# Kernel tuning notes

Hardware: AMD Instinct MI355X
Metric: run time of the kernel (lower is better)

The kernel has to match this reference:

```python
import jax, jax.numpy as jnp
import numpy as np

B = 1024
FEATURE_NUM = 13 + 26 * 4000  # 104013 (13 dense + 26 sparse fields, one-hot dim 4000 each)
FIELD_NUM = 13 + 26           # 39
K = 8


def setup_inputs() -> dict:
    key = jax.random.key(0)
    k1, k2, k3 = jax.random.split(key, 3)
    inputs = jax.random.uniform(k1, (B, FEATURE_NUM), dtype=jnp.float32)
    w0 = jnp.zeros((1,), dtype=jnp.float32)
    w = jax.random.normal(k2, (FEATURE_NUM, 1), dtype=jnp.float32) * 0.05
    v = jax.random.normal(k3, (FEATURE_NUM, FIELD_NUM, K), dtype=jnp.float32) * 0.05
    return {"inputs": inputs, "w0": w0, "w": w, "v": v}


def reference(inputs, w0, w, v):
    # linear part: [B, 1]
    linear_part = w0 + inputs @ w
    # field_f: [B, field_num, K] via tensordot over feature axis
    field_f = jnp.tensordot(inputs, v, axes=1)
    # sum over upper triangle (i<j) of <field_f_i, field_f_j> using the
    # sum-square FM identity: 0.5 * (||sum_i f_i||^2 - sum_i ||f_i||^2)
    s = field_f.sum(axis=1)                       # [B, K]
    inter = 0.5 * (jnp.sum(s * s, axis=-1)
                   - jnp.sum(field_f * field_f, axis=(1, 2)))  # [B]
    return linear_part + inter[:, None]           # [B, 1]
```

## Files before the change

kernel.cpp:

```cpp
#include <hip/hip_runtime.h>
#include <stdint.h>

#define B_SZ 1024
#define F_SZ 104013
#define NFIELD 39
#define N_RAW 312
#define N_PAD 320
#define KB_STEPS 3251
#define PART_ELEMS ((size_t)B_SZ * N_PAD)

using bf16x8 = __attribute__((ext_vector_type(8))) short;
using f32x4  = __attribute__((ext_vector_type(4))) float;

typedef __attribute__((address_space(3))) void* lds_vp;
typedef const __attribute__((address_space(1))) void* glb_cvp;

__device__ __forceinline__ void ld16(const void* g, void* l) {
  __builtin_amdgcn_global_load_lds((glb_cvp)g, (lds_vp)l, 16, 0, 0);
}

__device__ __forceinline__ unsigned int pack_bf16(float a, float b) {
  unsigned int ua = __float_as_uint(a) + 0x8000u;
  unsigned int ub = __float_as_uint(b) + 0x8000u;
  return (ua >> 16) | (ub & 0xffff0000u);
}

__global__ __launch_bounds__(256) void pack_v(const float* __restrict__ v,
                                              const float* __restrict__ w,
                                              uint4* __restrict__ Bp) {
  const int kb = blockIdx.x;
  const int t  = threadIdx.x;
  __shared__ float vs[32][324];

  for (int idx = t; idx < 32 * 78; idx += 256) {
    int r = idx / 78, c4 = (idx % 78) * 4;
    int k = kb * 32 + r;
    float4 val = make_float4(0.f, 0.f, 0.f, 0.f);
    if (k < F_SZ) val = *(const float4*)(v + (size_t)k * N_RAW + c4);
    *(float4*)&vs[r][c4] = val;
  }
  if (t < 32) {
    int k = kb * 32 + t;
    vs[t][312] = (k < F_SZ) ? w[k] : 0.f;
#pragma unroll
    for (int c = 313; c < 320; ++c) vs[t][c] = 0.f;
  }
  __syncthreads();

#pragma unroll
  for (int i = 0; i < 5; ++i) {
    int p  = t + 256 * i;
    int l  = p & 63;
    int kr = (l >> 4) * 8;
    int col = (p >> 6) * 16 + (l & 15);
    uint4 o;
    o.x = pack_bf16(vs[kr + 0][col], vs[kr + 1][col]);
    o.y = pack_bf16(vs[kr + 2][col], vs[kr + 3][col]);
    o.z = pack_bf16(vs[kr + 4][col], vs[kr + 5][col]);
    o.w = pack_bf16(vs[kr + 6][col], vs[kr + 7][col]);
    Bp[(size_t)kb * 1280 + p] = o;
  }
}

__global__ __launch_bounds__(256, 2) void gemm_split(const float* __restrict__ A,
                                                     const uint4* __restrict__ Bp,
                                                     float* __restrict__ part) {
  const int S  = gridDim.y;
  const int mt = blockIdx.x, s = blockIdx.y;
  const int t  = threadIdx.x;
  const int w  = t >> 6, l = t & 63;
  const int wr = w >> 1, wc = w & 1;
  const int lm = l & 15, lq = l >> 4;
  const int row0 = mt * 128;
  const int kb0 = (int)((long long)KB_STEPS * s / S);
  const int kb1 = (int)((long long)KB_STEPS * (s + 1) / S);

  __shared__ __align__(16) char smem[2][36864];

  const int lr  = l >> 3;
  const int kgl = ((l & 7) - lr) & 7;
  size_t arowbase[4];
#pragma unroll
  for (int j = 0; j < 4; ++j)
    arowbase[j] = (size_t)(row0 + (w * 4 + j) * 8 + lr) * F_SZ + (size_t)(kgl * 4);

  auto stage = [&](int kb, int buf, bool withA) {
    if (withA) {
#pragma unroll
      for (int j = 0; j < 4; ++j)
        ld16(A + arowbase[j] + (size_t)kb * 32, smem[buf] + (w * 4 + j) * 1024);
    }
#pragma unroll
    for (int j = 0; j < 5; ++j)
      ld16(Bp + ((size_t)kb * 20 + w * 5 + j) * 64 + l,
           smem[buf] + 16384 + (w * 5 + j) * 1024);
  };

  f32x4 acc[4][10];
#pragma unroll
  for (int i = 0; i < 4; ++i)
#pragma unroll
    for (int n = 0; n < 10; ++n) acc[i][n] = (f32x4)0.f;

  stage(kb0, 0, true);
  int cur = 0;
  for (int kb = kb0; kb < kb1; ++kb) {
    __syncthreads();
    if (kb + 1 < kb1) stage(kb + 1, cur ^ 1, (kb + 1) != KB_STEPS - 1);

    bf16x8 afrag[4];
    if (kb != KB_STEPS - 1) {
      const char* base = smem[cur];
      const int rot = lm & 7;
      const int p0 = (lq * 2 + rot) & 7;
      const int p1 = (lq * 2 + 1 + rot) & 7;
#pragma unroll
      for (int i = 0; i < 4; ++i) {
        int rowq = wr * 8 + i * 2 + (lm >> 3);
        f32x4 r0 = *(const f32x4*)(base + rowq * 1024 + rot * 128 + p0 * 16);
        f32x4 r1 = *(const f32x4*)(base + rowq * 1024 + rot * 128 + p1 * 16);
        uint4 pk = make_uint4(pack_bf16(r0[0], r0[1]), pack_bf16(r0[2], r0[3]),
                              pack_bf16(r1[0], r1[1]), pack_bf16(r1[2], r1[3]));
        afrag[i] = __builtin_bit_cast(bf16x8, pk);
      }
    } else {
      int kbase = kb * 32 + lq * 8;
#pragma unroll
      for (int i = 0; i < 4; ++i) {
        const float* ap = A + (size_t)(row0 + wr * 64 + i * 16 + lm) * F_SZ;
        float f[8];
#pragma unroll
        for (int jj = 0; jj < 8; ++jj)
          f[jj] = (kbase + jj < F_SZ) ? ap[kbase + jj] : 0.f;
        uint4 pk = make_uint4(pack_bf16(f[0], f[1]), pack_bf16(f[2], f[3]),
                              pack_bf16(f[4], f[5]), pack_bf16(f[6], f[7]));
        afrag[i] = __builtin_bit_cast(bf16x8, pk);
      }
    }

#pragma unroll
    for (int n = 0; n < 10; ++n) {
      bf16x8 bf = __builtin_bit_cast(
          bf16x8, *(const uint4*)(smem[cur] + 16384 + (wc * 10 + n) * 1024 + l * 16));
#pragma unroll
      for (int i = 0; i < 4; ++i)
        acc[i][n] = __builtin_amdgcn_mfma_f32_16x16x32_bf16(afrag[i], bf,
                                                            acc[i][n], 0, 0, 0);
    }
    cur ^= 1;
  }

  float* out = part + (size_t)s * PART_ELEMS;
#pragma unroll
  for (int i = 0; i < 4; ++i) {
    int rb = row0 + wr * 64 + i * 16 + lq * 4;
#pragma unroll
    for (int n = 0; n < 10; ++n) {
      int col = (wc * 10 + n) * 16 + lm;
#pragma unroll
      for (int r = 0; r < 4; ++r)
        out[(size_t)(rb + r) * N_PAD + col] = acc[i][n][r];
    }
  }
}

__global__ __launch_bounds__(256) void finalize(const float* __restrict__ part,
                                                const float* __restrict__ w0,
                                                float* __restrict__ out, int S) {
  const int b = blockIdx.x;
  const int t = threadIdx.x;
  __shared__ float crow[N_PAD];
  __shared__ float red[4];
  __shared__ float skl[8];

  for (int n = t; n < N_PAD; n += 256) {
    float acc = 0.f;
    for (int s = 0; s < S; ++s)
      acc += part[(size_t)s * PART_ELEMS + (size_t)b * N_PAD + n];
    crow[n] = acc;
  }
  __syncthreads();

  float sq = 0.f;
  for (int n = t; n < N_RAW; n += 256) sq += crow[n] * crow[n];
#pragma unroll
  for (int off = 32; off; off >>= 1) sq += __shfl_down(sq, off);
  if ((t & 63) == 0) red[t >> 6] = sq;
  if (t < 8) {
    float sk = 0.f;
#pragma unroll
    for (int f = 0; f < NFIELD; ++f) sk += crow[f * 8 + t];
    skl[t] = sk;
  }
  __syncthreads();
  if (t == 0) {
    float sumsq = red[0] + red[1] + red[2] + red[3];
    float ss = 0.f;
#pragma unroll
    for (int k = 0; k < 8; ++k) ss += skl[k] * skl[k];
    out[b] = w0[0] + crow[312] + 0.5f * (ss - sumsq);
  }
}

extern "C" void kernel_launch(void* const* d_in, const int* in_sizes, int n_in,
                              void* d_out, int out_size, void* d_ws, size_t ws_size,
                              hipStream_t stream) {
  const float* inputs = (const float*)d_in[0];
  const float* w0 = (const float*)d_in[1];
  const float* w  = (const float*)d_in[2];
  const float* v  = (const float*)d_in[3];
  float* out = (float*)d_out;

  const size_t PART_BYTES   = PART_ELEMS * sizeof(float);
  const size_t PACKED_BYTES = (size_t)KB_STEPS * 20 * 64 * 16;
  int S = 64;
  while (S > 1 && PACKED_BYTES + (size_t)S * PART_BYTES > ws_size) S >>= 1;

  float* part = (float*)d_ws;
  uint4* Bp   = (uint4*)((char*)d_ws + (size_t)S * PART_BYTES);

  pack_v<<<dim3(KB_STEPS), 256, 0, stream>>>(v, w, Bp);
  gemm_split<<<dim3(8, S), 256, 0, stream>>>(inputs, Bp, part);
  finalize<<<dim3(B_SZ), 256, 0, stream>>>(part, w0, out, S);
}
```

Before: 752.4 us.

## Convert A to bf16 during staging via register prefetch, widen GEMM blocks to 512 threads

The split-K GEMM now loads the A tile into registers two steps ahead, converts it to bf16 once, and writes it to a swizzled LDS layout. Previously fp32 went into LDS through direct global-to-LDS loads and every wave converted it again. Blocks grow to 8 waves with a 4-column wave split, LDS per buffer shrinks, the grid is reordered so split index is fastest, and the split count halves to 32. Finalize uses one thread per column and has fewer partials to sum. In exchange, register prefetch of A adds register pressure and gives up the asynchronous LDS load path for A.

```diff
diff --git a/kernel.cpp b/kernel.cpp
--- a/kernel.cpp
+++ b/kernel.cpp
@@ -62,130 +62,147 @@
   }
 }
 
-__global__ __launch_bounds__(256, 2) void gemm_split(const float* __restrict__ A,
+#define LDS_BUF 30720
+#define B_OFF   10240
+
+__global__ __launch_bounds__(512, 2) void gemm_split(const float* __restrict__ A,
                                                      const uint4* __restrict__ Bp,
                                                      float* __restrict__ part) {
-  const int S  = gridDim.y;
-  const int mt = blockIdx.x, s = blockIdx.y;
+  const int S  = gridDim.x;
+  const int s  = blockIdx.x, mt = blockIdx.y;
   const int t  = threadIdx.x;
   const int w  = t >> 6, l = t & 63;
-  const int wr = w >> 1, wc = w & 1;
+  const int wr = w >> 2, wc = w & 3;
   const int lm = l & 15, lq = l >> 4;
   const int row0 = mt * 128;
   const int kb0 = (int)((long long)KB_STEPS * s / S);
   const int kb1 = (int)((long long)KB_STEPS * (s + 1) / S);
 
-  __shared__ __align__(16) char smem[2][36864];
-
-  const int lr  = l >> 3;
-  const int kgl = ((l & 7) - lr) & 7;
-  size_t arowbase[4];
-#pragma unroll
-  for (int j = 0; j < 4; ++j)
-    arowbase[j] = (size_t)(row0 + (w * 4 + j) * 8 + lr) * F_SZ + (size_t)(kgl * 4);
-
-  auto stage = [&](int kb, int buf, bool withA) {
-    if (withA) {
-#pragma unroll
-      for (int j = 0; j < 4; ++j)
-        ld16(A + arowbase[j] + (size_t)kb * 32, smem[buf] + (w * 4 + j) * 1024);
-    }
-#pragma unroll
-    for (int j = 0; j < 5; ++j)
-      ld16(Bp + ((size_t)kb * 20 + w * 5 + j) * 64 + l,
-           smem[buf] + 16384 + (w * 5 + j) * 1024);
-  };
-
-  f32x4 acc[4][10];
+  __shared__ __align__(16) char smem[2][LDS_BUF];
+
+  const int srow = t >> 2, seg = t & 3;
+  const float* ag = A + (size_t)(row0 + srow) * F_SZ + seg * 8;
+  const int wswz = srow * 80 + ((seg ^ (srow & 3)) << 4);
+
+  auto loadA = [&](int kb, float4& d0, float4& d1) {
+    const float* ap = ag + (size_t)kb * 32;
+    if (kb != KB_STEPS - 1) {
+      d0 = *(const float4*)(ap);
+      d1 = *(const float4*)(ap + 4);
+    } else {
+      const int kbase = kb * 32 + seg * 8;
+      float f[8];
+#pragma unroll
+      for (int e = 0; e < 8; ++e) f[e] = (kbase + e < F_SZ) ? ap[e] : 0.f;
+      d0 = make_float4(f[0], f[1], f[2], f[3]);
+      d1 = make_float4(f[4], f[5], f[6], f[7]);
+    }
+  };
+
+  auto writeA = [&](int buf, const float4& d0, const float4& d1) {
+    uint4 pk;
+    pk.x = pack_bf16(d0.x, d0.y);
+    pk.y = pack_bf16(d0.z, d0.w);
+    pk.z = pack_bf16(d1.x, d1.y);
+    pk.w = pack_bf16(d1.z, d1.w);
+    *(uint4*)(smem[buf] + wswz) = pk;
+  };
+
+  auto stageB = [&](int kb, int buf) {
+    for (int c = w; c < 20; c += 8)
+      ld16(Bp + ((size_t)kb * 20 + c) * 64 + l, smem[buf] + B_OFF + c * 1024);
+  };
+
+  f32x4 acc[4][5];
 #pragma unroll
   for (int i = 0; i < 4; ++i)
 #pragma unroll
-    for (int n = 0; n < 10; ++n) acc[i][n] = (f32x4)0.f;
-
-  stage(kb0, 0, true);
-  int cur = 0;
-  for (int kb = kb0; kb < kb1; ++kb) {
+    for (int n = 0; n < 5; ++n) acc[i][n] = (f32x4)0.f;
+
+  auto compute = [&](int buf) {
+    const char* bs = smem[buf];
+    bf16x8 af[4];
+#pragma unroll
+    for (int i = 0; i < 4; ++i)
+      af[i] = __builtin_bit_cast(
+          bf16x8, *(const uint4*)(bs + (wr * 64 + i * 16 + lm) * 80 +
+                                  ((lq ^ (lm & 3)) << 4)));
+#pragma unroll
+    for (int n = 0; n < 5; ++n) {
+      bf16x8 bf = __builtin_bit_cast(
+          bf16x8, *(const uint4*)(bs + B_OFF + (wc * 5 + n) * 1024 + l * 16));
+#pragma unroll
+      for (int i = 0; i < 4; ++i)
+        acc[i][n] = __builtin_amdgcn_mfma_f32_16x16x32_bf16(af[i], bf,
+                                                            acc[i][n], 0, 0, 0);
+    }
+  };
+
+  float4 a0, a1, b0, b1;
+  loadA(kb0, a0, a1);
+  stageB(kb0, 0);
+  writeA(0, a0, a1);
+  if (kb0 + 1 < kb1) loadA(kb0 + 1, b0, b1);
+  __syncthreads();
+
+  int kb = kb0, cur = 0;
+  while (true) {
+    if (kb + 1 < kb1) {
+      stageB(kb + 1, cur ^ 1);
+      writeA(cur ^ 1, b0, b1);
+      if (kb + 2 < kb1) loadA(kb + 2, a0, a1);
+    }
+    compute(cur);
     __syncthreads();
-    if (kb + 1 < kb1) stage(kb + 1, cur ^ 1, (kb + 1) != KB_STEPS - 1);
-
-    bf16x8 afrag[4];
-    if (kb != KB_STEPS - 1) {
-      const char* base = smem[cur];
-      const int rot = lm & 7;
-      const int p0 = (lq * 2 + rot) & 7;
-      const int p1 = (lq * 2 + 1 + rot) & 7;
-#pragma unroll
-      for (int i = 0; i < 4; ++i) {
-        int rowq = wr * 8 + i * 2 + (lm >> 3);
-        f32x4 r0 = *(const f32x4*)(base + rowq * 1024 + rot * 128 + p0 * 16);
-        f32x4 r1 = *(const f32x4*)(base + rowq * 1024 + rot * 128 + p1 * 16);
-        uint4 pk = make_uint4(pack_bf16(r0[0], r0[1]), pack_bf16(r0[2], r0[3]),
-                              pack_bf16(r1[0], r1[1]), pack_bf16(r1[2], r1[3]));
-        afrag[i] = __builtin_bit_cast(bf16x8, pk);
-      }
-    } else {
-      int kbase = kb * 32 + lq * 8;
-#pragma unroll
-      for (int i = 0; i < 4; ++i) {
-        const float* ap = A + (size_t)(row0 + wr * 64 + i * 16 + lm) * F_SZ;
-        float f[8];
-#pragma unroll
-        for (int jj = 0; jj < 8; ++jj)
-          f[jj] = (kbase + jj < F_SZ) ? ap[kbase + jj] : 0.f;
-        uint4 pk = make_uint4(pack_bf16(f[0], f[1]), pack_bf16(f[2], f[3]),
-                              pack_bf16(f[4], f[5]), pack_bf16(f[6], f[7]));
-        afrag[i] = __builtin_bit_cast(bf16x8, pk);
-      }
-    }
-
-#pragma unroll
-    for (int n = 0; n < 10; ++n) {
-      bf16x8 bf = __builtin_bit_cast(
-          bf16x8, *(const uint4*)(smem[cur] + 16384 + (wc * 10 + n) * 1024 + l * 16));
-#pragma unroll
-      for (int i = 0; i < 4; ++i)
-        acc[i][n] = __builtin_amdgcn_mfma_f32_16x16x32_bf16(afrag[i], bf,
-                                                            acc[i][n], 0, 0, 0);
-    }
-    cur ^= 1;
-  }
-
-  float* out = part + (size_t)s * PART_ELEMS;
+    ++kb; cur ^= 1;
+    if (kb >= kb1) break;
+
+    if (kb + 1 < kb1) {
+      stageB(kb + 1, cur ^ 1);
+      writeA(cur ^ 1, a0, a1);
+      if (kb + 2 < kb1) loadA(kb + 2, b0, b1);
+    }
+    compute(cur);
+    __syncthreads();
+    ++kb; cur ^= 1;
+    if (kb >= kb1) break;
+  }
+
+  float* outp = part + (size_t)s * PART_ELEMS;
 #pragma unroll
   for (int i = 0; i < 4; ++i) {
     int rb = row0 + wr * 64 + i * 16 + lq * 4;
 #pragma unroll
-    for (int n = 0; n < 10; ++n) {
-      int col = (wc * 10 + n) * 16 + lm;
+    for (int n = 0; n < 5; ++n) {
+      int col = (wc * 5 + n) * 16 + lm;
 #pragma unroll
       for (int r = 0; r < 4; ++r)
-        out[(size_t)(rb + r) * N_PAD + col] = acc[i][n][r];
-    }
-  }
-}
-
-__global__ __launch_bounds__(256) void finalize(const float* __restrict__ part,
+        outp[(size_t)(rb + r) * N_PAD + col] = acc[i][n][r];
+    }
+  }
+}
+
+__global__ __launch_bounds__(320) void finalize(const float* __restrict__ part,
                                                 const float* __restrict__ w0,
                                                 float* __restrict__ out, int S) {
   const int b = blockIdx.x;
   const int t = threadIdx.x;
   __shared__ float crow[N_PAD];
-  __shared__ float red[4];
+  __shared__ float red[5];
   __shared__ float skl[8];
 
-  for (int n = t; n < N_PAD; n += 256) {
-    float acc = 0.f;
-    for (int s = 0; s < S; ++s)
-      acc += part[(size_t)s * PART_ELEMS + (size_t)b * N_PAD + n];
-    crow[n] = acc;
-  }
-  __syncthreads();
-
-  float sq = 0.f;
-  for (int n = t; n < N_RAW; n += 256) sq += crow[n] * crow[n];
+  float acc = 0.f;
+  const float* p = part + (size_t)b * N_PAD + t;
+#pragma unroll 4
+  for (int s = 0; s < S; ++s) acc += p[(size_t)s * PART_ELEMS];
+  crow[t] = acc;
+
+  float sq = (t < N_RAW) ? acc * acc : 0.f;
 #pragma unroll
   for (int off = 32; off; off >>= 1) sq += __shfl_down(sq, off);
   if ((t & 63) == 0) red[t >> 6] = sq;
+  __syncthreads();
+
   if (t < 8) {
     float sk = 0.f;
 #pragma unroll
@@ -194,7 +211,7 @@
   }
   __syncthreads();
   if (t == 0) {
-    float sumsq = red[0] + red[1] + red[2] + red[3];
+    float sumsq = red[0] + red[1] + red[2] + red[3] + red[4];
     float ss = 0.f;
 #pragma unroll
     for (int k = 0; k < 8; ++k) ss += skl[k] * skl[k];
@@ -213,13 +230,13 @@
 
   const size_t PART_BYTES   = PART_ELEMS * sizeof(float);
   const size_t PACKED_BYTES = (size_t)KB_STEPS * 20 * 64 * 16;
-  int S = 64;
+  int S = 32;
   while (S > 1 && PACKED_BYTES + (size_t)S * PART_BYTES > ws_size) S >>= 1;
 
   float* part = (float*)d_ws;
   uint4* Bp   = (uint4*)((char*)d_ws + (size_t)S * PART_BYTES);
 
   pack_v<<<dim3(KB_STEPS), 256, 0, stream>>>(v, w, Bp);
-  gemm_split<<<dim3(8, S), 256, 0, stream>>>(inputs, Bp, part);
-  finalize<<<dim3(B_SZ), 256, 0, stream>>>(part, w0, out, S);
-}
+  gemm_split<<<dim3(S, 8), 512, 0, stream>>>(inputs, Bp, part);
+  finalize<<<dim3(B_SZ), 320, 0, stream>>>(part, w0, out, S);
+}
```

After: 737.0 us. 2.1% less time.
